# Performance work log

Measured on AMD Instinct MI355X. Metric: run time of the kernel, lower is better.

## Reference

```python
import jax, jax.numpy as jnp
import numpy as np

N_NODES = 100_000
N_EDGES = 1_000_000
N_GRAPHS = 2048
F_IN, N_HEADS, HEAD_DIM = 128, 2, 32
NEG_SLOPE = 0.2


def seg_softmax(logits, seg, num):
    # numerically stable scatter-softmax over segments (leading axis)
    m = jax.ops.segment_max(logits, seg, num_segments=num)
    e = jnp.exp(logits - m[seg])
    s = jax.ops.segment_sum(e, seg, num_segments=num)
    return e / s[seg]


def setup_inputs() -> dict:
    key = jax.random.key(0)
    ks = jax.random.split(key, 10)
    HC = N_HEADS * HEAD_DIM
    x = jax.random.normal(ks[0], (N_NODES, F_IN), jnp.float32)
    edge_index = jax.random.randint(ks[1], (2, N_EDGES), 0, N_NODES, jnp.int32)
    batch = jnp.sort(jax.random.randint(ks[2], (N_NODES,), 0, N_GRAPHS, jnp.int32))
    sc_in = 1.0 / np.sqrt(F_IN)
    sc_hc = 1.0 / np.sqrt(HC)
    W_l = jax.random.normal(ks[3], (F_IN, HC), jnp.float32) * sc_in
    W_r = jax.random.normal(ks[4], (F_IN, HC), jnp.float32) * sc_in
    att = jax.random.normal(ks[5], (N_HEADS, HEAD_DIM), jnp.float32) * (1.0 / np.sqrt(HEAD_DIM))
    bias = jnp.zeros((HC,), jnp.float32)
    w_rel = jax.random.normal(ks[6], (HC,), jnp.float32) * sc_hc
    w_root = jax.random.normal(ks[7], (HC,), jnp.float32) * sc_hc
    b_score = jnp.zeros((1,), jnp.float32)
    return {"x": x, "edge_index": edge_index, "batch": batch, "W_l": W_l,
            "W_r": W_r, "att": att, "bias": bias, "w_rel": w_rel,
            "w_root": w_root, "b_score": b_score}


def reference(x, edge_index, batch, W_l, W_r, att, bias, w_rel, w_root, b_score):
    N = x.shape[0]
    H, C = att.shape
    src, dst = edge_index[0], edge_index[1]
    # --- GATv2Conv (add_self_loops=True, concat heads, negative_slope=0.2) ---
    loop = jnp.arange(N, dtype=src.dtype)
    s = jnp.concatenate([src, loop])  # source j
    d = jnp.concatenate([dst, loop])  # target i
    xl = (x @ W_l).reshape(N, H, C)   # lin_l -> source features
    xr = (x @ W_r).reshape(N, H, C)   # lin_r -> target features
    e = jax.nn.leaky_relu(xl[s] + xr[d], NEG_SLOPE)       # [E', H, C]
    logits = jnp.einsum('ehc,hc->eh', e, att)              # [E', H]
    alpha = seg_softmax(logits, d, N)                      # softmax over incoming edges per target
    h = jax.ops.segment_sum(xl[s] * alpha[:, :, None], d, num_segments=N)
    h = h.reshape(N, H * C) + bias                         # conv output (data.x)
    # --- SAGPooling(min_score=-1): softmax(GraphConv score) keeps all nodes ---
    aggr = jax.ops.segment_sum(h[src], dst, num_segments=N)  # GraphConv neighbor add-aggr
    score = aggr @ w_rel + h @ w_root + b_score              # [N]
    sm = seg_softmax(score, batch, N_GRAPHS)
    px = h * sm[:, None]
    # --- global_add_pool + global_mean_pool ---
    add = jax.ops.segment_sum(px, batch, num_segments=N_GRAPHS)
    cnt = jax.ops.segment_sum(jnp.ones((N,), px.dtype), batch, num_segments=N_GRAPHS)
    mean = add / jnp.maximum(cnt, 1.0)[:, None]
    return add + mean  # global_emb [N_GRAPHS, H*C]
```

## Files before the change

### kernel.cpp

```cpp
#include <hip/hip_runtime.h>
#include <hip/hip_bf16.h>

#define N_NODES 100000
#define N_EDGES 1000000
#define N_GRAPHS 2048
#define F_IN 128
#define NEG_SLOPE 0.2f
#define E_TOT (N_EDGES + N_NODES)
#define GEMM_BLOCKS 782
#define NODE_BLOCKS 391
#define NB 1563
#define EB 269
#define EB_PAD 272
#define CPW_BLOCKS 391

typedef short  bf16x8 __attribute__((ext_vector_type(8)));
typedef float  f32x16 __attribute__((ext_vector_type(16)));

__device__ __forceinline__ short f2bf(float f) {
    unsigned u = __float_as_uint(f);
    unsigned r = (u + 0x7fffu + ((u >> 16) & 1u)) >> 16;
    return (short)r;
}
__device__ __forceinline__ float bf2f(short h) {
    return __uint_as_float(((unsigned)(unsigned short)h) << 16);
}

template <int CTRL>
__device__ __forceinline__ float dpp_add(float x) {
    return x + __int_as_float(__builtin_amdgcn_update_dpp(
        0, __float_as_int(x), CTRL, 0xf, 0xf, true));
}
__device__ __forceinline__ float head_sum_bcast(float x) {
    x = dpp_add<0x111>(x);
    x = dpp_add<0x112>(x);
    x = dpp_add<0x114>(x);
    x = dpp_add<0x118>(x);
    x = dpp_add<0x142>(x);
    return __int_as_float(__builtin_amdgcn_ds_swizzle(__float_as_int(x), 0x03E0));
}
__device__ __forceinline__ float full_sum64(float x) {
    x = dpp_add<0x111>(x);
    x = dpp_add<0x112>(x);
    x = dpp_add<0x114>(x);
    x = dpp_add<0x118>(x);
    x = dpp_add<0x142>(x);
    x = dpp_add<0x143>(x);
    return x;
}
__device__ __forceinline__ float quad_sum(float x) {
    x = dpp_add<0xB1>(x);
    x = dpp_add<0x4E>(x);
    return x;
}

__global__ __launch_bounds__(256) void k_gemm(const float* __restrict__ x,
                                              const float* __restrict__ Wl,
                                              const float* __restrict__ Wr,
                                              float* __restrict__ xlr) {
    __shared__ short wt[2][128][136];
    int tid = threadIdx.x;
    {
        int k  = tid >> 1;
        int cq = tid & 1;
        const float* Wsrc = cq ? Wr : Wl;
#pragma unroll
        for (int u = 0; u < 16; ++u) {
            int c0 = u * 4;
            float4 wv = *(const float4*)(Wsrc + (size_t)k * 64 + c0);
            float vv[4] = {wv.x, wv.y, wv.z, wv.w};
#pragma unroll
            for (int q = 0; q < 4; ++q) {
                int c = cq * 64 + c0 + q;
                short hi = f2bf(vv[q]);
                wt[0][c][k] = hi;
                wt[1][c][k] = f2bf(vv[q] - bf2f(hi));
            }
        }
    }
    __syncthreads();
    int lane = tid & 63, w = tid >> 6;
    int m = lane & 31, half = lane >> 5;
    int row = blockIdx.x * 128 + w * 32 + m;
    bool rv = row < N_NODES;
    const float* xrow = x + (size_t)(rv ? row : 0) * F_IN;
    f32x16 acc[4];
#pragma unroll
    for (int t = 0; t < 4; ++t)
#pragma unroll
        for (int i = 0; i < 16; ++i) acc[t][i] = 0.f;

#pragma unroll
    for (int kt = 0; kt < 8; ++kt) {
        int kb = kt * 16 + half * 8;
        float4 xa = rv ? *(const float4*)(xrow + kb)
                       : make_float4(0.f, 0.f, 0.f, 0.f);
        float4 xb = rv ? *(const float4*)(xrow + kb + 4)
                       : make_float4(0.f, 0.f, 0.f, 0.f);
        float xs[8] = {xa.x, xa.y, xa.z, xa.w, xb.x, xb.y, xb.z, xb.w};
        bf16x8 ahi, alo;
#pragma unroll
        for (int j = 0; j < 8; ++j) {
            short hi = f2bf(xs[j]);
            ahi[j] = hi;
            alo[j] = f2bf(xs[j] - bf2f(hi));
        }
#pragma unroll
        for (int t = 0; t < 4; ++t) {
            int n = t * 32 + m;
            bf16x8 bhi = *(const bf16x8*)&wt[0][n][kb];
            bf16x8 blo = *(const bf16x8*)&wt[1][n][kb];
            acc[t] = __builtin_amdgcn_mfma_f32_32x32x16_bf16(ahi, bhi, acc[t], 0, 0, 0);
            acc[t] = __builtin_amdgcn_mfma_f32_32x32x16_bf16(ahi, blo, acc[t], 0, 0, 0);
            acc[t] = __builtin_amdgcn_mfma_f32_32x32x16_bf16(alo, bhi, acc[t], 0, 0, 0);
        }
    }
    int r0 = blockIdx.x * 128 + w * 32 + 4 * half;
#pragma unroll
    for (int t = 0; t < 4; ++t)
#pragma unroll
        for (int reg = 0; reg < 16; ++reg) {
            int rr = r0 + (reg & 3) + 8 * (reg >> 2);
            if (rr < N_NODES)
                xlr[(size_t)rr * 128 + t * 32 + m] = acc[t][reg];
        }
}

__global__ __launch_bounds__(256) void k_bhist(const int* __restrict__ ei,
                                               int* __restrict__ bhist) {
    __shared__ int lh[NB];
    int tid = threadIdx.x, b = blockIdx.x;
    for (int i = tid; i < NB; i += 256) lh[i] = 0;
    __syncthreads();
    int e0 = b * 4096;
#pragma unroll
    for (int j = 0; j < 16; ++j) {
        int e = e0 + j * 256 + tid;
        if (e < E_TOT) {
            int d = (e < N_EDGES) ? ei[N_EDGES + e] : (e - N_EDGES);
            atomicAdd(&lh[d >> 6], 1);
        }
    }
    __syncthreads();
    for (int i = tid; i < NB; i += 256)
        bhist[(size_t)i * EB_PAD + b] = lh[i];
}

__global__ __launch_bounds__(256) void k_colprefix_bounds(int* __restrict__ bhist,
                                                          int* __restrict__ colsum,
                                                          const int* __restrict__ batch,
                                                          int* __restrict__ start) {
    if (blockIdx.x < CPW_BLOCKS) {
        int wv = blockIdx.x * 4 + (threadIdx.x >> 6);
        if (wv >= NB) return;
        int lane = threadIdx.x & 63;
        int* row = bhist + (size_t)wv * EB_PAD;
        int carry = 0;
        for (int base = 0; base < EB; base += 64) {
            int idx = base + lane;
            int v = (idx < EB) ? row[idx] : 0;
            int inc = v;
#pragma unroll
            for (int o = 1; o < 64; o <<= 1) {
                int t = __shfl_up(inc, o, 64);
                if (lane >= o) inc += t;
            }
            int tot = __shfl(inc, 63, 64);
            if (idx < EB) row[idx] = carry + inc - v;
            carry += tot;
        }
        if (lane == 0) colsum[wv] = carry;
    } else {
        int i = (blockIdx.x - CPW_BLOCKS) * 256 + threadIdx.x;
        if (i >= N_NODES) return;
        int bi = batch[i];
        int bp = (i == 0) ? -1 : batch[i - 1];
        for (int g = bp + 1; g <= bi; ++g) start[g] = i;
        if (i == N_NODES - 1)
            for (int g = bi + 1; g <= N_GRAPHS; ++g) start[g] = N_NODES;
    }
}

__global__ __launch_bounds__(256) void k_cbscan(const int* __restrict__ colsum,
                                                int* __restrict__ colbase) {
    __shared__ int sh[256];
    int t = threadIdx.x;
    int v[7]; int s = 0;
#pragma unroll
    for (int k = 0; k < 7; ++k) {
        int idx = t * 7 + k;
        v[k] = (idx < NB) ? colsum[idx] : 0;
        s += v[k];
    }
    sh[t] = s; __syncthreads();
    for (int off = 1; off < 256; off <<= 1) {
        int xv = (t >= off) ? sh[t - off] : 0;
        __syncthreads();
        sh[t] += xv;
        __syncthreads();
    }
    int run = sh[t] - s;
#pragma unroll
    for (int k = 0; k < 7; ++k) {
        int idx = t * 7 + k;
        if (idx <= NB) colbase[idx] = run;
        run += v[k];
    }
}

__global__ __launch_bounds__(256) void k_bscatter(const int* __restrict__ ei,
                                                  const int* __restrict__ bhist,
                                                  const int* __restrict__ colbase,
                                                  int* __restrict__ bpack) {
    __shared__ int lh[NB];
    int tid = threadIdx.x, b = blockIdx.x;
    for (int i = tid; i < NB; i += 256) lh[i] = 0;
    __syncthreads();
    int e0 = b * 4096;
#pragma unroll
    for (int j = 0; j < 16; ++j) {
        int e = e0 + j * 256 + tid;
        if (e < E_TOT) {
            int s, d;
            if (e < N_EDGES) { s = ei[e]; d = ei[N_EDGES + e]; }
            else             { s = d = e - N_EDGES; }
            int bk = d >> 6;
            int lr = atomicAdd(&lh[bk], 1);
            int pos = colbase[bk] + bhist[(size_t)bk * EB_PAD + b] + lr;
            bpack[pos] = s | ((d & 63) << 17);
        }
    }
}

__global__ __launch_bounds__(256) void k_fine(const int* __restrict__ bpack,
                                              const int* __restrict__ colbase,
                                              int* __restrict__ rowptr,
                                              int* __restrict__ sorted_src) {
    __shared__ int fcnt[64];
    __shared__ int foff[64];
    int i = blockIdx.x, tid = threadIdx.x;
    int cb0 = colbase[i], cb1 = colbase[i + 1];
    if (tid < 64) fcnt[tid] = 0;
    __syncthreads();
    for (int e = cb0 + tid; e < cb1; e += 256)
        atomicAdd(&fcnt[bpack[e] >> 17], 1);
    __syncthreads();
    if (tid < 64) {
        int v = fcnt[tid];
        int inc = v;
#pragma unroll
        for (int o = 1; o < 64; o <<= 1) {
            int t = __shfl_up(inc, o, 64);
            if (tid >= o) inc += t;
        }
        int excl = inc - v;
        foff[tid] = excl;
        int node = i * 64 + tid;
        if (node <= N_NODES) rowptr[node] = cb0 + excl;
    }
    __syncthreads();
    for (int e = cb0 + tid; e < cb1; e += 256) {
        int w = bpack[e];
        int lr = atomicAdd(&foff[w >> 17], 1);
        sorted_src[cb0 + lr] = w & 131071;
    }
}

__global__ __launch_bounds__(256) void k_gat(const float* __restrict__ xlr,
                                             const int* __restrict__ rowptr,
                                             const int* __restrict__ sorted_src,
                                             const float* __restrict__ att,
                                             const float* __restrict__ bias,
                                             const float* __restrict__ w_rel,
                                             const float* __restrict__ w_root,
                                             float* __restrict__ hfeat,
                                             float* __restrict__ tbuf,
                                             float* __restrict__ rbuf) {
    int lane = threadIdx.x & 63;
    int du = __builtin_amdgcn_readfirstlane(blockIdx.x * 4 + (threadIdx.x >> 6));
    if (du >= N_NODES) return;
    float xr_l  = xlr[(size_t)du * 128 + 64 + lane];
    float att_l = att[lane];
    int j0 = __builtin_amdgcn_readfirstlane(rowptr[du]);
    int j1 = __builtin_amdgcn_readfirstlane(rowptr[du + 1]);
    float wsum = 0.f, acc = 0.f;
    int jc = j0;
    for (; jc + 8 <= j1; jc += 8) {
        int sv = sorted_src[jc + (lane & 7)];
        float p[8], xv[8];
#pragma unroll
        for (int i = 0; i < 8; ++i) {
            int s = __builtin_amdgcn_readlane(sv, i);
            xv[i] = (xlr + (size_t)(unsigned)s * 128)[lane];
        }
#pragma unroll
        for (int i = 0; i < 8; ++i) {
            float v = xv[i] + xr_l;
            v = (v > 0.f) ? v : NEG_SLOPE * v;
            p[i] = v * att_l;
        }
#pragma unroll
        for (int i = 0; i < 8; ++i)
            p[i] = head_sum_bcast(p[i]);
#pragma unroll
        for (int i = 0; i < 8; ++i) {
            float w = __expf(p[i]);
            wsum += w;
            acc += w * xv[i];
        }
    }
    for (; jc < j1; jc += 4) {
        int n = j1 - jc;
        int jj = jc + (lane & 3);
        if (jj > j1 - 1) jj = j1 - 1;
        int sv = sorted_src[jj];
        float p[4], xv[4];
#pragma unroll
        for (int i = 0; i < 4; ++i) {
            int s = __builtin_amdgcn_readlane(sv, i);
            xv[i] = (xlr + (size_t)(unsigned)s * 128)[lane];
        }
#pragma unroll
        for (int i = 0; i < 4; ++i) {
            float v = xv[i] + xr_l;
            v = (v > 0.f) ? v : NEG_SLOPE * v;
            p[i] = v * att_l;
        }
#pragma unroll
        for (int i = 0; i < 4; ++i)
            p[i] = head_sum_bcast(p[i]);
#pragma unroll
        for (int i = 0; i < 4; ++i) {
            float w = (i < n) ? __expf(p[i]) : 0.f;
            wsum += w;
            acc += w * xv[i];
        }
    }
    float h = acc / wsum + bias[lane];
    hfeat[(size_t)du * 64 + lane] = h;
    float a = full_sum64(h * w_rel[lane]);
    float b = full_sum64(h * w_root[lane]);
    if (lane == 63) { tbuf[du] = a; rbuf[du] = b; }
}

__global__ __launch_bounds__(256) void k_pool(const int* __restrict__ rowptr,
                                              const int* __restrict__ sorted_src,
                                              const float* __restrict__ t,
                                              const float* __restrict__ r,
                                              const float* __restrict__ b_score,
                                              float* __restrict__ score,
                                              const float* __restrict__ h,
                                              const int* __restrict__ start,
                                              float* __restrict__ out) {
    __shared__ float sh[4];
    __shared__ float shacc[4][64];
    int g = blockIdx.x;
    int tid = threadIdx.x, w = tid >> 6, lane = tid & 63;
    int n0 = start[g], n1 = start[g + 1];
    int cnt = n1 - n0;
    if (cnt <= 0) { if (tid < 64) out[(size_t)g * 64 + tid] = 0.f; return; }
    float bsc = b_score[0];
    for (int base = n0; base < n1; base += 64) {
        int i = base + (tid >> 2);
        float sum = 0.f;
        int jj0 = 0, jj1 = 0;
        if (i < n1) { jj0 = rowptr[i]; jj1 = rowptr[i + 1]; }
        for (int j = jj0 + (tid & 3); j < jj1; j += 4)
            sum += t[sorted_src[j]];
        sum = quad_sum(sum);
        if (i < n1 && (tid & 3) == 0)
            score[i] = sum - t[i] + r[i] + bsc;
    }
    __syncthreads();
    float m = -1e30f;
    for (int i = n0 + tid; i < n1; i += 256) m = fmaxf(m, score[i]);
#pragma unroll
    for (int o = 32; o; o >>= 1) m = fmaxf(m, __shfl_xor(m, o, 64));
    if (lane == 0) sh[w] = m;
    __syncthreads();
    m = fmaxf(fmaxf(sh[0], sh[1]), fmaxf(sh[2], sh[3]));
    float ssum = 0.f;
    for (int i = n0 + tid; i < n1; i += 256) ssum += __expf(score[i] - m);
#pragma unroll
    for (int o = 32; o; o >>= 1) ssum += __shfl_xor(ssum, o, 64);
    __syncthreads();
    if (lane == 0) sh[w] = ssum;
    __syncthreads();
    ssum = sh[0] + sh[1] + sh[2] + sh[3];
    float acc = 0.f;
    for (int i = n0 + w; i < n1; i += 4)
        acc += __expf(score[i] - m) * h[(size_t)i * 64 + lane];
    shacc[w][lane] = acc;
    __syncthreads();
    if (w == 0) {
        float tot = shacc[0][lane] + shacc[1][lane] + shacc[2][lane] + shacc[3][lane];
        out[(size_t)g * 64 + lane] = tot * (1.f + 1.f / (float)cnt) / ssum;
    }
}

extern "C" void kernel_launch(void* const* d_in, const int* in_sizes, int n_in,
                              void* d_out, int out_size, void* d_ws, size_t ws_size,
                              hipStream_t stream) {
    const float* x      = (const float*)d_in[0];
    const int*   ei     = (const int*)d_in[1];
    const int*   batch  = (const int*)d_in[2];
    const float* Wl     = (const float*)d_in[3];
    const float* Wr     = (const float*)d_in[4];
    const float* att    = (const float*)d_in[5];
    const float* bias   = (const float*)d_in[6];
    const float* w_rel  = (const float*)d_in[7];
    const float* w_root = (const float*)d_in[8];
    const float* b_sc   = (const float*)d_in[9];

    char* ws = (char*)d_ws;
    size_t off = 0;
    auto alloc = [&](size_t bytes) { void* p = ws + off; off += (bytes + 255) & ~255ull; return p; };
    float* xlr        = (float*)alloc((size_t)N_NODES * 128 * 4);
    float* hfeat      = (float*)alloc((size_t)N_NODES * 64 * 4);
    int*   bhist      = (int*)hfeat;
    int*   bpack      = (int*)  alloc((size_t)E_TOT * 4);
    int*   sorted_src = (int*)  alloc((size_t)E_TOT * 4);
    int*   rowptr     = (int*)  alloc((size_t)(N_NODES + 1) * 4);
    int*   colsum     = (int*)  alloc((size_t)NB * 4);
    int*   colbase    = (int*)  alloc((size_t)(NB + 1) * 4);
    float* tbuf       = (float*)alloc((size_t)N_NODES * 4);
    float* rbuf       = (float*)alloc((size_t)N_NODES * 4);
    float* score      = (float*)alloc((size_t)N_NODES * 4);
    int*   start      = (int*)  alloc((size_t)(N_GRAPHS + 1) * 4);

    k_gemm            <<<GEMM_BLOCKS, 256, 0, stream>>>(x, Wl, Wr, xlr);
    k_bhist           <<<EB, 256, 0, stream>>>(ei, bhist);
    k_colprefix_bounds<<<CPW_BLOCKS + NODE_BLOCKS, 256, 0, stream>>>(bhist, colsum, batch, start);
    k_cbscan          <<<1, 256, 0, stream>>>(colsum, colbase);
    k_bscatter        <<<EB, 256, 0, stream>>>(ei, bhist, colbase, bpack);
    k_fine            <<<NB, 256, 0, stream>>>(bpack, colbase, rowptr, sorted_src);
    k_gat             <<<(N_NODES + 3) / 4, 256, 0, stream>>>(xlr, rowptr, sorted_src, att, bias,
                                                              w_rel, w_root, hfeat, tbuf, rbuf);
    k_pool            <<<N_GRAPHS, 256, 0, stream>>>(rowptr, sorted_src, tbuf, rbuf, b_sc,
                                                     score, hfeat, start, (float*)d_out);
}
```

Before: 243.9 us.

## Fuse GEMM with histogram, scan into scatter, and fine sort into GAT

Merges the bf16 GEMM and the edge bucket histogram into one launch, and has every scatter block recompute the column prefix scan instead of running a separate single-block kernel. The fine per-bucket sort is fused with GAT aggregation, keeping sorted sources in LDS and having each block process its 64 destination nodes. The pool kernel caches exp scores to avoid recomputing them. This removes three kernel launches and some global traffic. The cost is less parallelism in the GAT stage (four waves per 64 nodes) and a fixed LDS capacity for edges per bucket.

```diff
diff --git a/kernel.cpp b/kernel.cpp
--- a/kernel.cpp
+++ b/kernel.cpp
@@ -13,6 +13,7 @@
 #define EB 269
 #define EB_PAD 272
 #define CPW_BLOCKS 391
+#define SLDS_CAP 1088
 
 typedef short  bf16x8 __attribute__((ext_vector_type(8)));
 typedef float  f32x16 __attribute__((ext_vector_type(16)));
@@ -54,12 +55,35 @@
     return x;
 }
 
-__global__ __launch_bounds__(256) void k_gemm(const float* __restrict__ x,
-                                              const float* __restrict__ Wl,
-                                              const float* __restrict__ Wr,
-                                              float* __restrict__ xlr) {
-    __shared__ short wt[2][128][136];
+__global__ __launch_bounds__(256) void k_gemm_bhist(const float* __restrict__ x,
+                                                    const float* __restrict__ Wl,
+                                                    const float* __restrict__ Wr,
+                                                    const int* __restrict__ ei,
+                                                    float* __restrict__ xlr,
+                                                    int* __restrict__ bhist) {
+    __shared__ unsigned char smem[2 * 128 * 136 * 2];
     int tid = threadIdx.x;
+    if (blockIdx.x >= GEMM_BLOCKS) {
+        int* lh = (int*)smem;
+        int b = blockIdx.x - GEMM_BLOCKS;
+        for (int i = tid; i < NB; i += 256) lh[i] = 0;
+        __syncthreads();
+        int e0 = b * 4096;
+#pragma unroll
+        for (int j = 0; j < 16; ++j) {
+            int e = e0 + j * 256 + tid;
+            if (e < E_TOT) {
+                int d = (e < N_EDGES) ? ei[N_EDGES + e] : (e - N_EDGES);
+                atomicAdd(&lh[d >> 6], 1);
+            }
+        }
+        __syncthreads();
+        for (int i = tid; i < NB; i += 256)
+            bhist[(size_t)i * EB_PAD + b] = lh[i];
+        return;
+    }
+    typedef short wt_t[128][136];
+    wt_t* wt = (wt_t*)smem;
     {
         int k  = tid >> 1;
         int cq = tid & 1;
@@ -124,26 +148,6 @@
             if (rr < N_NODES)
                 xlr[(size_t)rr * 128 + t * 32 + m] = acc[t][reg];
         }
-}
-
-__global__ __launch_bounds__(256) void k_bhist(const int* __restrict__ ei,
-                                               int* __restrict__ bhist) {
-    __shared__ int lh[NB];
-    int tid = threadIdx.x, b = blockIdx.x;
-    for (int i = tid; i < NB; i += 256) lh[i] = 0;
-    __syncthreads();
-    int e0 = b * 4096;
-#pragma unroll
-    for (int j = 0; j < 16; ++j) {
-        int e = e0 + j * 256 + tid;
-        if (e < E_TOT) {
-            int d = (e < N_EDGES) ? ei[N_EDGES + e] : (e - N_EDGES);
-            atomicAdd(&lh[d >> 6], 1);
-        }
-    }
-    __syncthreads();
-    for (int i = tid; i < NB; i += 256)
-        bhist[(size_t)i * EB_PAD + b] = lh[i];
 }
 
 __global__ __launch_bounds__(256) void k_colprefix_bounds(int* __restrict__ bhist,
@@ -181,41 +185,42 @@
     }
 }
 
-__global__ __launch_bounds__(256) void k_cbscan(const int* __restrict__ colsum,
-                                                int* __restrict__ colbase) {
-    __shared__ int sh[256];
-    int t = threadIdx.x;
-    int v[7]; int s = 0;
-#pragma unroll
-    for (int k = 0; k < 7; ++k) {
-        int idx = t * 7 + k;
-        v[k] = (idx < NB) ? colsum[idx] : 0;
-        s += v[k];
-    }
-    sh[t] = s; __syncthreads();
-    for (int off = 1; off < 256; off <<= 1) {
-        int xv = (t >= off) ? sh[t - off] : 0;
-        __syncthreads();
-        sh[t] += xv;
-        __syncthreads();
-    }
-    int run = sh[t] - s;
-#pragma unroll
-    for (int k = 0; k < 7; ++k) {
-        int idx = t * 7 + k;
-        if (idx <= NB) colbase[idx] = run;
-        run += v[k];
-    }
-}
-
 __global__ __launch_bounds__(256) void k_bscatter(const int* __restrict__ ei,
                                                   const int* __restrict__ bhist,
-                                                  const int* __restrict__ colbase,
+                                                  const int* __restrict__ colsum,
+                                                  int* __restrict__ colbase,
                                                   int* __restrict__ bpack) {
     __shared__ int lh[NB];
+    __shared__ int cb[NB + 1];
+    __shared__ int sctmp[256];
     int tid = threadIdx.x, b = blockIdx.x;
+    {
+        int v[7]; int s = 0;
+#pragma unroll
+        for (int k = 0; k < 7; ++k) {
+            int idx = tid * 7 + k;
+            v[k] = (idx < NB) ? colsum[idx] : 0;
+            s += v[k];
+        }
+        sctmp[tid] = s; __syncthreads();
+        for (int off = 1; off < 256; off <<= 1) {
+            int xv = (tid >= off) ? sctmp[tid - off] : 0;
+            __syncthreads();
+            sctmp[tid] += xv;
+            __syncthreads();
+        }
+        int run = sctmp[tid] - s;
+#pragma unroll
+        for (int k = 0; k < 7; ++k) {
+            int idx = tid * 7 + k;
+            if (idx <= NB) cb[idx] = run;
+            run += v[k];
+        }
+    }
     for (int i = tid; i < NB; i += 256) lh[i] = 0;
     __syncthreads();
+    if (b == 0)
+        for (int i = tid; i <= NB; i += 256) colbase[i] = cb[i];
     int e0 = b * 4096;
 #pragma unroll
     for (int j = 0; j < 16; ++j) {
@@ -226,24 +231,35 @@
             else             { s = d = e - N_EDGES; }
             int bk = d >> 6;
             int lr = atomicAdd(&lh[bk], 1);
-            int pos = colbase[bk] + bhist[(size_t)bk * EB_PAD + b] + lr;
+            int pos = cb[bk] + bhist[(size_t)bk * EB_PAD + b] + lr;
             bpack[pos] = s | ((d & 63) << 17);
         }
     }
 }
 
-__global__ __launch_bounds__(256) void k_fine(const int* __restrict__ bpack,
-                                              const int* __restrict__ colbase,
-                                              int* __restrict__ rowptr,
-                                              int* __restrict__ sorted_src) {
+__global__ __launch_bounds__(256) void k_gatfine(const float* __restrict__ xlr,
+                                                 const int* __restrict__ bpack,
+                                                 const int* __restrict__ colbase,
+                                                 const float* __restrict__ att,
+                                                 const float* __restrict__ bias,
+                                                 const float* __restrict__ w_rel,
+                                                 const float* __restrict__ w_root,
+                                                 int* __restrict__ rowptr,
+                                                 int* __restrict__ sorted_src,
+                                                 float* __restrict__ hfeat,
+                                                 float* __restrict__ tbuf,
+                                                 float* __restrict__ rbuf) {
+    __shared__ int lrp[65];
     __shared__ int fcnt[64];
     __shared__ int foff[64];
-    int i = blockIdx.x, tid = threadIdx.x;
-    int cb0 = colbase[i], cb1 = colbase[i + 1];
+    __shared__ int slds[SLDS_CAP];
+    int bi = blockIdx.x, tid = threadIdx.x;
+    int cb0 = colbase[bi], cb1 = colbase[bi + 1];
+    int cnt = cb1 - cb0;
     if (tid < 64) fcnt[tid] = 0;
     __syncthreads();
-    for (int e = cb0 + tid; e < cb1; e += 256)
-        atomicAdd(&fcnt[bpack[e] >> 17], 1);
+    for (int e = tid; e < cnt; e += 256)
+        atomicAdd(&fcnt[bpack[cb0 + e] >> 17], 1);
     __syncthreads();
     if (tid < 64) {
         int v = fcnt[tid];
@@ -255,92 +271,91 @@
         }
         int excl = inc - v;
         foff[tid] = excl;
-        int node = i * 64 + tid;
+        lrp[tid] = excl;
+        if (tid == 63) lrp[64] = inc;
+        int node = bi * 64 + tid;
         if (node <= N_NODES) rowptr[node] = cb0 + excl;
     }
     __syncthreads();
-    for (int e = cb0 + tid; e < cb1; e += 256) {
-        int w = bpack[e];
+    for (int e = tid; e < cnt; e += 256) {
+        int w = bpack[cb0 + e];
         int lr = atomicAdd(&foff[w >> 17], 1);
-        sorted_src[cb0 + lr] = w & 131071;
-    }
-}
-
-__global__ __launch_bounds__(256) void k_gat(const float* __restrict__ xlr,
-                                             const int* __restrict__ rowptr,
-                                             const int* __restrict__ sorted_src,
-                                             const float* __restrict__ att,
-                                             const float* __restrict__ bias,
-                                             const float* __restrict__ w_rel,
-                                             const float* __restrict__ w_root,
-                                             float* __restrict__ hfeat,
-                                             float* __restrict__ tbuf,
-                                             float* __restrict__ rbuf) {
-    int lane = threadIdx.x & 63;
-    int du = __builtin_amdgcn_readfirstlane(blockIdx.x * 4 + (threadIdx.x >> 6));
-    if (du >= N_NODES) return;
-    float xr_l  = xlr[(size_t)du * 128 + 64 + lane];
-    float att_l = att[lane];
-    int j0 = __builtin_amdgcn_readfirstlane(rowptr[du]);
-    int j1 = __builtin_amdgcn_readfirstlane(rowptr[du + 1]);
-    float wsum = 0.f, acc = 0.f;
-    int jc = j0;
-    for (; jc + 8 <= j1; jc += 8) {
-        int sv = sorted_src[jc + (lane & 7)];
-        float p[8], xv[8];
-#pragma unroll
-        for (int i = 0; i < 8; ++i) {
-            int s = __builtin_amdgcn_readlane(sv, i);
-            xv[i] = (xlr + (size_t)(unsigned)s * 128)[lane];
-        }
-#pragma unroll
-        for (int i = 0; i < 8; ++i) {
-            float v = xv[i] + xr_l;
-            v = (v > 0.f) ? v : NEG_SLOPE * v;
-            p[i] = v * att_l;
-        }
-#pragma unroll
-        for (int i = 0; i < 8; ++i)
-            p[i] = head_sum_bcast(p[i]);
-#pragma unroll
-        for (int i = 0; i < 8; ++i) {
-            float w = __expf(p[i]);
-            wsum += w;
-            acc += w * xv[i];
-        }
-    }
-    for (; jc < j1; jc += 4) {
-        int n = j1 - jc;
-        int jj = jc + (lane & 3);
-        if (jj > j1 - 1) jj = j1 - 1;
-        int sv = sorted_src[jj];
-        float p[4], xv[4];
-#pragma unroll
-        for (int i = 0; i < 4; ++i) {
-            int s = __builtin_amdgcn_readlane(sv, i);
-            xv[i] = (xlr + (size_t)(unsigned)s * 128)[lane];
-        }
-#pragma unroll
-        for (int i = 0; i < 4; ++i) {
-            float v = xv[i] + xr_l;
-            v = (v > 0.f) ? v : NEG_SLOPE * v;
-            p[i] = v * att_l;
-        }
-#pragma unroll
-        for (int i = 0; i < 4; ++i)
-            p[i] = head_sum_bcast(p[i]);
-#pragma unroll
-        for (int i = 0; i < 4; ++i) {
-            float w = (i < n) ? __expf(p[i]) : 0.f;
-            wsum += w;
-            acc += w * xv[i];
-        }
-    }
-    float h = acc / wsum + bias[lane];
-    hfeat[(size_t)du * 64 + lane] = h;
-    float a = full_sum64(h * w_rel[lane]);
-    float b = full_sum64(h * w_root[lane]);
-    if (lane == 63) { tbuf[du] = a; rbuf[du] = b; }
+        int s = w & 131071;
+        slds[lr] = s;
+        sorted_src[cb0 + lr] = s;
+    }
+    __syncthreads();
+    int lane = tid & 63, wv = tid >> 6;
+    float att_l  = att[lane];
+    float bias_l = bias[lane];
+    float wrel_l = w_rel[lane];
+    float wroot_l = w_root[lane];
+    for (int q = 0; q < 16; ++q) {
+        int dl = wv * 16 + q;
+        int du = bi * 64 + dl;
+        if (du >= N_NODES) break;
+        int j0 = __builtin_amdgcn_readfirstlane(lrp[dl]);
+        int j1 = __builtin_amdgcn_readfirstlane(lrp[dl + 1]);
+        float xr_l = xlr[(size_t)du * 128 + 64 + lane];
+        float wsum = 0.f, acc = 0.f;
+        int jc = j0;
+        for (; jc + 8 <= j1; jc += 8) {
+            int sv = slds[jc + (lane & 7)];
+            float p[8], xv[8];
+#pragma unroll
+            for (int i = 0; i < 8; ++i) {
+                int s = __builtin_amdgcn_readlane(sv, i);
+                xv[i] = (xlr + (size_t)(unsigned)s * 128)[lane];
+            }
+#pragma unroll
+            for (int i = 0; i < 8; ++i) {
+                float v = xv[i] + xr_l;
+                v = (v > 0.f) ? v : NEG_SLOPE * v;
+                p[i] = v * att_l;
+            }
+#pragma unroll
+            for (int i = 0; i < 8; ++i)
+                p[i] = head_sum_bcast(p[i]);
+#pragma unroll
+            for (int i = 0; i < 8; ++i) {
+                float w = __expf(p[i]);
+                wsum += w;
+                acc += w * xv[i];
+            }
+        }
+        for (; jc < j1; jc += 4) {
+            int n = j1 - jc;
+            int jj = jc + (lane & 3);
+            if (jj > j1 - 1) jj = j1 - 1;
+            int sv = slds[jj];
+            float p[4], xv[4];
+#pragma unroll
+            for (int i = 0; i < 4; ++i) {
+                int s = __builtin_amdgcn_readlane(sv, i);
+                xv[i] = (xlr + (size_t)(unsigned)s * 128)[lane];
+            }
+#pragma unroll
+            for (int i = 0; i < 4; ++i) {
+                float v = xv[i] + xr_l;
+                v = (v > 0.f) ? v : NEG_SLOPE * v;
+                p[i] = v * att_l;
+            }
+#pragma unroll
+            for (int i = 0; i < 4; ++i)
+                p[i] = head_sum_bcast(p[i]);
+#pragma unroll
+            for (int i = 0; i < 4; ++i) {
+                float w = (i < n) ? __expf(p[i]) : 0.f;
+                wsum += w;
+                acc += w * xv[i];
+            }
+        }
+        float h = acc / wsum + bias_l;
+        hfeat[(size_t)du * 64 + lane] = h;
+        float a = full_sum64(h * wrel_l);
+        float b = full_sum64(h * wroot_l);
+        if (lane == 63) { tbuf[du] = a; rbuf[du] = b; }
+    }
 }
 
 __global__ __launch_bounds__(256) void k_pool(const int* __restrict__ rowptr,
@@ -379,17 +394,21 @@
     if (lane == 0) sh[w] = m;
     __syncthreads();
     m = fmaxf(fmaxf(sh[0], sh[1]), fmaxf(sh[2], sh[3]));
+    __syncthreads();
     float ssum = 0.f;
-    for (int i = n0 + tid; i < n1; i += 256) ssum += __expf(score[i] - m);
+    for (int i = n0 + tid; i < n1; i += 256) {
+        float e = __expf(score[i] - m);
+        score[i] = e;
+        ssum += e;
+    }
 #pragma unroll
     for (int o = 32; o; o >>= 1) ssum += __shfl_xor(ssum, o, 64);
-    __syncthreads();
     if (lane == 0) sh[w] = ssum;
     __syncthreads();
     ssum = sh[0] + sh[1] + sh[2] + sh[3];
     float acc = 0.f;
     for (int i = n0 + w; i < n1; i += 4)
-        acc += __expf(score[i] - m) * h[(size_t)i * 64 + lane];
+        acc += score[i] * h[(size_t)i * 64 + lane];
     shacc[w][lane] = acc;
     __syncthreads();
     if (w == 0) {
@@ -428,14 +447,11 @@
     float* score      = (float*)alloc((size_t)N_NODES * 4);
     int*   start      = (int*)  alloc((size_t)(N_GRAPHS + 1) * 4);
 
-    k_gemm            <<<GEMM_BLOCKS, 256, 0, stream>>>(x, Wl, Wr, xlr);
-    k_bhist           <<<EB, 256, 0, stream>>>(ei, bhist);
+    k_gemm_bhist      <<<GEMM_BLOCKS + EB, 256, 0, stream>>>(x, Wl, Wr, ei, xlr, bhist);
     k_colprefix_bounds<<<CPW_BLOCKS + NODE_BLOCKS, 256, 0, stream>>>(bhist, colsum, batch, start);
-    k_cbscan          <<<1, 256, 0, stream>>>(colsum, colbase);
-    k_bscatter        <<<EB, 256, 0, stream>>>(ei, bhist, colbase, bpack);
-    k_fine            <<<NB, 256, 0, stream>>>(bpack, colbase, rowptr, sorted_src);
-    k_gat             <<<(N_NODES + 3) / 4, 256, 0, stream>>>(xlr, rowptr, sorted_src, att, bias,
-                                                              w_rel, w_root, hfeat, tbuf, rbuf);
+    k_bscatter        <<<EB, 256, 0, stream>>>(ei, bhist, colsum, colbase, bpack);
+    k_gatfine         <<<NB, 256, 0, stream>>>(xlr, bpack, colbase, att, bias, w_rel, w_root,
+                                               rowptr, sorted_src, hfeat, tbuf, rbuf);
     k_pool            <<<N_GRAPHS, 256, 0, stream>>>(rowptr, sorted_src, tbuf, rbuf, b_sc,
                                                      score, hfeat, start, (float*)d_out);
 }
```

New measurement: 239.0 us. 2.0% less time.

## Fuse GEMM with histogram, fold column scan into scatter, prefetch GAT gathers

Applied to the files above, without the earlier changes.

The edge-bucket histogram now runs as extra blocks inside the GEMM launch, and the single-block column-sum scan is recomputed redundantly in every scatter block, with block 0 writing colbase. This removes two kernel launches and their serialization. The GAT aggregation loop is restructured to software-pipeline the next 8 neighbor gathers while computing the current ones, and replaces the 4-wide tail loop with masked 8-wide processing. The pooling kernel caches exp(score-m) in the score buffer instead of recomputing it. Each scatter block now repeats the same scan, and the prefetch raises register pressure in GAT.

```diff
diff --git a/kernel.cpp b/kernel.cpp
--- a/kernel.cpp
+++ b/kernel.cpp
@@ -54,12 +54,35 @@
     return x;
 }
 
-__global__ __launch_bounds__(256) void k_gemm(const float* __restrict__ x,
-                                              const float* __restrict__ Wl,
-                                              const float* __restrict__ Wr,
-                                              float* __restrict__ xlr) {
-    __shared__ short wt[2][128][136];
+__global__ __launch_bounds__(256) void k_gemm_bhist(const float* __restrict__ x,
+                                                    const float* __restrict__ Wl,
+                                                    const float* __restrict__ Wr,
+                                                    const int* __restrict__ ei,
+                                                    float* __restrict__ xlr,
+                                                    int* __restrict__ bhist) {
+    __shared__ unsigned char smem[2 * 128 * 136 * 2];
     int tid = threadIdx.x;
+    if (blockIdx.x >= GEMM_BLOCKS) {
+        int* lh = (int*)smem;
+        int b = blockIdx.x - GEMM_BLOCKS;
+        for (int i = tid; i < NB; i += 256) lh[i] = 0;
+        __syncthreads();
+        int e0 = b * 4096;
+#pragma unroll
+        for (int j = 0; j < 16; ++j) {
+            int e = e0 + j * 256 + tid;
+            if (e < E_TOT) {
+                int d = (e < N_EDGES) ? ei[N_EDGES + e] : (e - N_EDGES);
+                atomicAdd(&lh[d >> 6], 1);
+            }
+        }
+        __syncthreads();
+        for (int i = tid; i < NB; i += 256)
+            bhist[(size_t)i * EB_PAD + b] = lh[i];
+        return;
+    }
+    typedef short wt_t[128][136];
+    wt_t* wt = (wt_t*)smem;
     {
         int k  = tid >> 1;
         int cq = tid & 1;
@@ -124,26 +147,6 @@
             if (rr < N_NODES)
                 xlr[(size_t)rr * 128 + t * 32 + m] = acc[t][reg];
         }
-}
-
-__global__ __launch_bounds__(256) void k_bhist(const int* __restrict__ ei,
-                                               int* __restrict__ bhist) {
-    __shared__ int lh[NB];
-    int tid = threadIdx.x, b = blockIdx.x;
-    for (int i = tid; i < NB; i += 256) lh[i] = 0;
-    __syncthreads();
-    int e0 = b * 4096;
-#pragma unroll
-    for (int j = 0; j < 16; ++j) {
-        int e = e0 + j * 256 + tid;
-        if (e < E_TOT) {
-            int d = (e < N_EDGES) ? ei[N_EDGES + e] : (e - N_EDGES);
-            atomicAdd(&lh[d >> 6], 1);
-        }
-    }
-    __syncthreads();
-    for (int i = tid; i < NB; i += 256)
-        bhist[(size_t)i * EB_PAD + b] = lh[i];
 }
 
 __global__ __launch_bounds__(256) void k_colprefix_bounds(int* __restrict__ bhist,
@@ -181,41 +184,42 @@
     }
 }
 
-__global__ __launch_bounds__(256) void k_cbscan(const int* __restrict__ colsum,
-                                                int* __restrict__ colbase) {
-    __shared__ int sh[256];
-    int t = threadIdx.x;
-    int v[7]; int s = 0;
-#pragma unroll
-    for (int k = 0; k < 7; ++k) {
-        int idx = t * 7 + k;
-        v[k] = (idx < NB) ? colsum[idx] : 0;
-        s += v[k];
-    }
-    sh[t] = s; __syncthreads();
-    for (int off = 1; off < 256; off <<= 1) {
-        int xv = (t >= off) ? sh[t - off] : 0;
-        __syncthreads();
-        sh[t] += xv;
-        __syncthreads();
-    }
-    int run = sh[t] - s;
-#pragma unroll
-    for (int k = 0; k < 7; ++k) {
-        int idx = t * 7 + k;
-        if (idx <= NB) colbase[idx] = run;
-        run += v[k];
-    }
-}
-
 __global__ __launch_bounds__(256) void k_bscatter(const int* __restrict__ ei,
                                                   const int* __restrict__ bhist,
-                                                  const int* __restrict__ colbase,
+                                                  const int* __restrict__ colsum,
+                                                  int* __restrict__ colbase,
                                                   int* __restrict__ bpack) {
     __shared__ int lh[NB];
+    __shared__ int cb[NB + 1];
+    __shared__ int sctmp[256];
     int tid = threadIdx.x, b = blockIdx.x;
+    {
+        int v[7]; int s = 0;
+#pragma unroll
+        for (int k = 0; k < 7; ++k) {
+            int idx = tid * 7 + k;
+            v[k] = (idx < NB) ? colsum[idx] : 0;
+            s += v[k];
+        }
+        sctmp[tid] = s; __syncthreads();
+        for (int off = 1; off < 256; off <<= 1) {
+            int xv = (tid >= off) ? sctmp[tid - off] : 0;
+            __syncthreads();
+            sctmp[tid] += xv;
+            __syncthreads();
+        }
+        int run = sctmp[tid] - s;
+#pragma unroll
+        for (int k = 0; k < 7; ++k) {
+            int idx = tid * 7 + k;
+            if (idx <= NB) cb[idx] = run;
+            run += v[k];
+        }
+    }
     for (int i = tid; i < NB; i += 256) lh[i] = 0;
     __syncthreads();
+    if (b == 0)
+        for (int i = tid; i <= NB; i += 256) colbase[i] = cb[i];
     int e0 = b * 4096;
 #pragma unroll
     for (int j = 0; j < 16; ++j) {
@@ -226,7 +230,7 @@
             else             { s = d = e - N_EDGES; }
             int bk = d >> 6;
             int lr = atomicAdd(&lh[bk], 1);
-            int pos = colbase[bk] + bhist[(size_t)bk * EB_PAD + b] + lr;
+            int pos = cb[bk] + bhist[(size_t)bk * EB_PAD + b] + lr;
             bpack[pos] = s | ((d & 63) << 17);
         }
     }
@@ -285,14 +289,33 @@
     int j1 = __builtin_amdgcn_readfirstlane(rowptr[du + 1]);
     float wsum = 0.f, acc = 0.f;
     int jc = j0;
-    for (; jc + 8 <= j1; jc += 8) {
-        int sv = sorted_src[jc + (lane & 7)];
-        float p[8], xv[8];
+    float xv[8];
+    {
+        int jj = jc + (lane & 7);
+        if (jj > j1 - 1) jj = j1 - 1;
+        int sv = sorted_src[jj];
 #pragma unroll
         for (int i = 0; i < 8; ++i) {
             int s = __builtin_amdgcn_readlane(sv, i);
             xv[i] = (xlr + (size_t)(unsigned)s * 128)[lane];
         }
+    }
+    while (true) {
+        int n = j1 - jc;
+        int jn = jc + 8;
+        bool more = jn < j1;
+        float xvn[8];
+        if (more) {
+            int jj = jn + (lane & 7);
+            if (jj > j1 - 1) jj = j1 - 1;
+            int sv = sorted_src[jj];
+#pragma unroll
+            for (int i = 0; i < 8; ++i) {
+                int s = __builtin_amdgcn_readlane(sv, i);
+                xvn[i] = (xlr + (size_t)(unsigned)s * 128)[lane];
+            }
+        }
+        float p[8];
 #pragma unroll
         for (int i = 0; i < 8; ++i) {
             float v = xv[i] + xr_l;
@@ -302,39 +325,25 @@
 #pragma unroll
         for (int i = 0; i < 8; ++i)
             p[i] = head_sum_bcast(p[i]);
-#pragma unroll
-        for (int i = 0; i < 8; ++i) {
-            float w = __expf(p[i]);
-            wsum += w;
-            acc += w * xv[i];
-        }
-    }
-    for (; jc < j1; jc += 4) {
-        int n = j1 - jc;
-        int jj = jc + (lane & 3);
-        if (jj > j1 - 1) jj = j1 - 1;
-        int sv = sorted_src[jj];
-        float p[4], xv[4];
-#pragma unroll
-        for (int i = 0; i < 4; ++i) {
-            int s = __builtin_amdgcn_readlane(sv, i);
-            xv[i] = (xlr + (size_t)(unsigned)s * 128)[lane];
-        }
-#pragma unroll
-        for (int i = 0; i < 4; ++i) {
-            float v = xv[i] + xr_l;
-            v = (v > 0.f) ? v : NEG_SLOPE * v;
-            p[i] = v * att_l;
-        }
-#pragma unroll
-        for (int i = 0; i < 4; ++i)
-            p[i] = head_sum_bcast(p[i]);
-#pragma unroll
-        for (int i = 0; i < 4; ++i) {
-            float w = (i < n) ? __expf(p[i]) : 0.f;
-            wsum += w;
-            acc += w * xv[i];
-        }
+        if (n >= 8) {
+#pragma unroll
+            for (int i = 0; i < 8; ++i) {
+                float w = __expf(p[i]);
+                wsum += w;
+                acc += w * xv[i];
+            }
+        } else {
+#pragma unroll
+            for (int i = 0; i < 8; ++i) {
+                float w = (i < n) ? __expf(p[i]) : 0.f;
+                wsum += w;
+                acc += w * xv[i];
+            }
+        }
+        if (!more) break;
+        jc = jn;
+#pragma unroll
+        for (int i = 0; i < 8; ++i) xv[i] = xvn[i];
     }
     float h = acc / wsum + bias[lane];
     hfeat[(size_t)du * 64 + lane] = h;
@@ -379,17 +388,21 @@
     if (lane == 0) sh[w] = m;
     __syncthreads();
     m = fmaxf(fmaxf(sh[0], sh[1]), fmaxf(sh[2], sh[3]));
+    __syncthreads();
     float ssum = 0.f;
-    for (int i = n0 + tid; i < n1; i += 256) ssum += __expf(score[i] - m);
+    for (int i = n0 + tid; i < n1; i += 256) {
+        float e = __expf(score[i] - m);
+        score[i] = e;
+        ssum += e;
+    }
 #pragma unroll
     for (int o = 32; o; o >>= 1) ssum += __shfl_xor(ssum, o, 64);
-    __syncthreads();
     if (lane == 0) sh[w] = ssum;
     __syncthreads();
     ssum = sh[0] + sh[1] + sh[2] + sh[3];
     float acc = 0.f;
     for (int i = n0 + w; i < n1; i += 4)
-        acc += __expf(score[i] - m) * h[(size_t)i * 64 + lane];
+        acc += score[i] * h[(size_t)i * 64 + lane];
     shacc[w][lane] = acc;
     __syncthreads();
     if (w == 0) {
@@ -428,11 +441,9 @@
     float* score      = (float*)alloc((size_t)N_NODES * 4);
     int*   start      = (int*)  alloc((size_t)(N_GRAPHS + 1) * 4);
 
-    k_gemm            <<<GEMM_BLOCKS, 256, 0, stream>>>(x, Wl, Wr, xlr);
-    k_bhist           <<<EB, 256, 0, stream>>>(ei, bhist);
+    k_gemm_bhist      <<<GEMM_BLOCKS + EB, 256, 0, stream>>>(x, Wl, Wr, ei, xlr, bhist);
     k_colprefix_bounds<<<CPW_BLOCKS + NODE_BLOCKS, 256, 0, stream>>>(bhist, colsum, batch, start);
-    k_cbscan          <<<1, 256, 0, stream>>>(colsum, colbase);
-    k_bscatter        <<<EB, 256, 0, stream>>>(ei, bhist, colbase, bpack);
+    k_bscatter        <<<EB, 256, 0, stream>>>(ei, bhist, colsum, colbase, bpack);
     k_fine            <<<NB, 256, 0, stream>>>(bpack, colbase, rowptr, sorted_src);
     k_gat             <<<(N_NODES + 3) / 4, 256, 0, stream>>>(xlr, rowptr, sorted_src, att, bias,
                                                               w_rel, w_root, hfeat, tbuf, rbuf);
```

After: 238.0 us. -2.4%, faster.
